# Optimization experiments

Hardware: AMD Instinct MI355X
Metric: run time of the kernel (lower is better)

The kernel has to match this reference:

```python
import jax, jax.numpy as jnp
import numpy as np

NUM_EXPERTS = 8
IN_FEATURES = 1024
OUT_FEATURES = 1024
TOTAL_TOKENS = 8192


def setup_inputs() -> dict:
    key = jax.random.key(0)
    k_x, k_w, k_b = jax.random.split(key, 3)
    inputs = jax.random.normal(k_x, (TOTAL_TOKENS, IN_FEATURES), dtype=jnp.float32)
    # lecun_normal-style scale for the per-expert kernels
    kernel = jax.random.normal(k_w, (NUM_EXPERTS, IN_FEATURES, OUT_FEATURES), dtype=jnp.float32) / np.sqrt(IN_FEATURES)
    bias = jax.random.normal(k_b, (NUM_EXPERTS, OUT_FEATURES), dtype=jnp.float32) * 0.01
    # ragged group sizes that sum exactly to TOTAL_TOKENS (tokens pre-sorted by expert)
    rng = np.random.default_rng(0)
    gs = rng.multinomial(TOTAL_TOKENS, [1.0 / NUM_EXPERTS] * NUM_EXPERTS)
    group_sizes = jnp.asarray(gs, dtype=jnp.int32)
    return {"inputs": inputs, "group_sizes": group_sizes, "kernel": kernel, "bias": bias}


def reference(inputs, group_sizes, kernel, bias):
    # inputs: [T, in], kernel: [E, in, out], bias: [E, out], group_sizes: [E]
    E = kernel.shape[0]
    T = inputs.shape[0]
    # per-token expert id (tokens are sorted/grouped by expert)
    expert_ids = jnp.repeat(jnp.arange(E, dtype=jnp.int32), group_sizes, total_repeat_length=T)  # [T]
    onehot = jax.nn.one_hot(expert_ids, E, dtype=inputs.dtype)  # [T, E]
    # grouped ragged matmul: y[t] = x[t] @ W[expert_ids[t]]
    xe = jnp.einsum("te,ti->eti", onehot, inputs)  # [E, T, in], zero outside each expert's group
    y = jnp.einsum("eti,eio->to", xe, kernel)  # [T, out]
    # ragged bias expansion: bias of the owning expert per token
    y = y + jnp.take(bias, expert_ids, axis=0)
    return y
```

## Files before the change

### kernel.cpp

```cpp
#include <hip/hip_runtime.h>
#include <hip/hip_bf16.h>

#define KDIM 1024
#define NDIM 1024
#define NEXP 8
#define TTOK 8192

typedef __bf16 bf16x8 __attribute__((ext_vector_type(8)));
typedef __bf16 bf16x4 __attribute__((ext_vector_type(4)));
typedef float  f32x4  __attribute__((ext_vector_type(4)));

__device__ __forceinline__ void gl2lds16(const void* g, void* l) {
  __builtin_amdgcn_global_load_lds(
      (const __attribute__((address_space(1))) void*)g,
      (__attribute__((address_space(3))) void*)l, 16, 0, 0);
}


__global__ __launch_bounds__(256) void prepass(
    const float* __restrict__ x, const float* __restrict__ W,
    __bf16* __restrict__ swA, __bf16* __restrict__ swB)
{
  __shared__ __align__(16) __bf16 Lt[64 * 72];
  const int t = threadIdx.x;
  if (blockIdx.x < 1024) {
#pragma unroll
    for (int p = 0; p < 4; ++p) {
      int s = blockIdx.x * 1024 + p * 256 + t;
      int lane = s & 63, kt = (s >> 6) & 31, panel = s >> 11;
      int row = panel * 16 + (lane & 15);
      int k0 = kt * 32 + ((lane >> 4) << 3);
      const float* xp = x + (size_t)row * KDIM + k0;
      float4 a = *(const float4*)xp;
      float4 b = *(const float4*)(xp + 4);
      bf16x8 v;
      v[0] = (__bf16)a.x; v[1] = (__bf16)a.y; v[2] = (__bf16)a.z; v[3] = (__bf16)a.w;
      v[4] = (__bf16)b.x; v[5] = (__bf16)b.y; v[6] = (__bf16)b.z; v[7] = (__bf16)b.w;
      *(bf16x8*)(swA + (size_t)s * 8) = v;
    }
  } else {
    int bid = blockIdx.x - 1024;
    int e = bid >> 8, r = bid & 255;
    int k0 = (r >> 4) * 64, n0 = (r & 15) * 64;
    const float* Wp = W + (size_t)e * KDIM * NDIM;
    int rr0 = t >> 4, c4 = t & 15;
#pragma unroll
    for (int p = 0; p < 4; ++p) {
      int kk = rr0 + p * 16;
      float4 v = *(const float4*)(Wp + (size_t)(k0 + kk) * NDIM + n0 + c4 * 4);
      Lt[(c4 * 4 + 0) * 72 + kk] = (__bf16)v.x;
      Lt[(c4 * 4 + 1) * 72 + kk] = (__bf16)v.y;
      Lt[(c4 * 4 + 2) * 72 + kk] = (__bf16)v.z;
      Lt[(c4 * 4 + 3) * 72 + kk] = (__bf16)v.w;
    }
    __syncthreads();
#pragma unroll
    for (int q = 0; q < 2; ++q) {
      int slot = q * 256 + t;
      int lane = slot & 63, grp = slot >> 6;
      int np = grp & 3, kt2 = grp >> 2;
      int nl = np * 16 + (lane & 15);
      int kl = kt2 * 32 + ((lane >> 4) << 3);
      bf16x8 v = *(const bf16x8*)(Lt + nl * 72 + kl);
      int panel = (n0 >> 4) + np;
      int ktg = (k0 >> 5) + kt2;
      size_t sg = (((size_t)e * 64 + panel) * 32 + ktg) * 64 + lane;
      *(bf16x8*)(swB + sg * 8) = v;
    }
  }
}

__global__ __launch_bounds__(256, 3) void moe_gemm_lds(
    const __bf16* __restrict__ swA, const __bf16* __restrict__ swB,
    const int* __restrict__ gs, const float* __restrict__ bias,
    float* __restrict__ out)
{
  __shared__ __align__(16) __bf16 buf[3][8192];

  int y = blockIdx.y;
  int e = 0, tile0 = 0, lo = 0, hi = 0, found = 0, off = 0;
#pragma unroll
  for (int i = 0; i < NEXP; ++i) {
    int g = gs[i];
    int first = off >> 7;
    int cnt = (g > 0) ? (((off + g - 1) >> 7) - first + 1) : 0;
    if (!found) {
      if (y < cnt) {
        found = 1; e = i; tile0 = (first + y) << 7;
        lo = max(tile0, off); hi = min(tile0 + 128, off + g);
      } else y -= cnt;
    }
    off += g;
  }
  if (!found) return;
  const int n0 = blockIdx.x * 128;

  const int t = threadIdx.x, lane = t & 63, wv = t >> 6;
  const int wm = wv & 1, wn = wv >> 1, lm = lane & 15, lg = lane >> 4;

  const __bf16* gA0 = swA + (size_t)((tile0 >> 4) + wv) * 16384 + lane * 8;
  const __bf16* gA1 = swA + (size_t)((tile0 >> 4) + 4 + wv) * 16384 + lane * 8;
  const __bf16* gB0 = swB + (size_t)(e * 64 + (n0 >> 4) + wv) * 16384 + lane * 8;
  const __bf16* gB1 = swB + (size_t)(e * 64 + (n0 >> 4) + 4 + wv) * 16384 + lane * 8;

  auto stage = [&](int kt, int sb) {
    __bf16* l = &buf[sb][0];
    const int ko = kt * 512;
    gl2lds16(gA0 + ko, l + (size_t)(0 * 256 + wv * 64) * 8);
    gl2lds16(gA1 + ko, l + (size_t)(1 * 256 + wv * 64) * 8);
    gl2lds16(gB0 + ko, l + (size_t)(2 * 256 + wv * 64) * 8);
    gl2lds16(gB1 + ko, l + (size_t)(3 * 256 + wv * 64) * 8);
  };

  f32x4 acc[4][4] = {};
  auto compute = [&](const __bf16* l) {
    bf16x8 aF[4], bF[4];
#pragma unroll
    for (int i = 0; i < 4; ++i)
      aF[i] = *(const bf16x8*)(l + (size_t)((wm * 4 + i) * 64 + lane) * 8);
#pragma unroll
    for (int j = 0; j < 4; ++j)
      bF[j] = *(const bf16x8*)(l + 4096 + (size_t)((wn * 4 + j) * 64 + lane) * 8);
#pragma unroll
    for (int i = 0; i < 4; ++i)
#pragma unroll
      for (int j = 0; j < 4; ++j)
        acc[i][j] = __builtin_amdgcn_mfma_f32_16x16x32_bf16(aF[i], bF[j], acc[i][j], 0, 0, 0);
  };

  stage(0, 0);
  stage(1, 1);
#pragma unroll 1
  for (int kt = 0; kt < KDIM / 32 - 1; ++kt) {
    asm volatile("s_waitcnt vmcnt(4)" ::: "memory");
    asm volatile("s_barrier" ::: "memory");
    compute(&buf[kt % 3][0]);
    if (kt + 2 < KDIM / 32) stage(kt + 2, (kt + 2) % 3);
  }
  asm volatile("s_waitcnt vmcnt(0)" ::: "memory");
  asm volatile("s_barrier" ::: "memory");
  compute(&buf[(KDIM / 32 - 1) % 3][0]);

  float bj[4];
#pragma unroll
  for (int j = 0; j < 4; ++j) bj[j] = bias[e * NDIM + n0 + wn * 64 + j * 16 + lm];
#pragma unroll
  for (int i = 0; i < 4; ++i)
#pragma unroll
    for (int r = 0; r < 4; ++r) {
      int rabs = tile0 + wm * 64 + i * 16 + lg * 4 + r;
      if (rabs >= lo && rabs < hi) {
#pragma unroll
        for (int j = 0; j < 4; ++j)
          out[(size_t)rabs * NDIM + n0 + wn * 64 + j * 16 + lm] = acc[i][j][r] + bj[j];
      }
    }
}

#define LDA 40
__global__ __launch_bounds__(256) void moe_gemm_kernel(
    const float* __restrict__ x, const int* __restrict__ gs,
    const float* __restrict__ W, const float* __restrict__ bias,
    float* __restrict__ out)
{
  __shared__ __bf16 Al[128 * LDA];
  __shared__ __bf16 Bl[128 * LDA];
  const int e = blockIdx.z, mt = blockIdx.y, nt = blockIdx.x;
  int off = 0;
#pragma unroll
  for (int i = 0; i < NEXP; ++i) { int g = gs[i]; if (i < e) off += g; }
  const int ge = gs[e];
  const int m0 = mt * 128;
  if (m0 >= ge) return;
  const int rows = min(128, ge - m0);
  const int row0 = off + m0;
  const int n0 = nt * 128;
  const int t = threadIdx.x, lane = t & 63, wv = t >> 6;
  const int wm = wv & 1, wn = wv >> 1, lm = lane & 15, lg = lane >> 4;
  const int am = t >> 3, kq = t & 7, nb = t & 127, kh = t >> 7;
  float4 aReg[4]; float bReg[16];
  const float* Wp = W + (size_t)e * KDIM * NDIM + n0 + nb;
  auto load_tile = [&](int kt) {
#pragma unroll
    for (int p = 0; p < 4; ++p) {
      int r = am + 32 * p;
      if (r < rows) aReg[p] = *(const float4*)(x + (size_t)(row0 + r) * KDIM + kt * 32 + kq * 4);
      else aReg[p] = make_float4(0.f, 0.f, 0.f, 0.f);
    }
    const float* wp = Wp + (size_t)(kt * 32 + kh * 16) * NDIM;
#pragma unroll
    for (int j = 0; j < 16; ++j) bReg[j] = wp[(size_t)j * NDIM];
  };
  auto store_tile = [&]() {
#pragma unroll
    for (int p = 0; p < 4; ++p) {
      bf16x4 v;
      v[0] = (__bf16)aReg[p].x; v[1] = (__bf16)aReg[p].y;
      v[2] = (__bf16)aReg[p].z; v[3] = (__bf16)aReg[p].w;
      *(bf16x4*)(Al + (am + 32 * p) * LDA + kq * 4) = v;
    }
    bf16x8 b0, b1;
#pragma unroll
    for (int j = 0; j < 8; ++j) { b0[j] = (__bf16)bReg[j]; b1[j] = (__bf16)bReg[8 + j]; }
    *(bf16x8*)(Bl + nb * LDA + kh * 16) = b0;
    *(bf16x8*)(Bl + nb * LDA + kh * 16 + 8) = b1;
  };
  f32x4 acc[4][4] = {};
  load_tile(0);
#pragma unroll 1
  for (int kt = 0; kt < KDIM / 32; ++kt) {
    __syncthreads();
    store_tile();
    __syncthreads();
    if (kt + 1 < KDIM / 32) load_tile(kt + 1);
    bf16x8 af[4], bfr[4];
#pragma unroll
    for (int i = 0; i < 4; ++i)
      af[i] = *(const bf16x8*)(Al + (wm * 64 + i * 16 + lm) * LDA + lg * 8);
#pragma unroll
    for (int j = 0; j < 4; ++j)
      bfr[j] = *(const bf16x8*)(Bl + (wn * 64 + j * 16 + lm) * LDA + lg * 8);
#pragma unroll
    for (int i = 0; i < 4; ++i)
#pragma unroll
      for (int j = 0; j < 4; ++j)
        acc[i][j] = __builtin_amdgcn_mfma_f32_16x16x32_bf16(af[i], bfr[j], acc[i][j], 0, 0, 0);
  }
  float bj[4];
#pragma unroll
  for (int j = 0; j < 4; ++j) bj[j] = bias[e * NDIM + n0 + wn * 64 + j * 16 + lm];
#pragma unroll
  for (int i = 0; i < 4; ++i)
#pragma unroll
    for (int r = 0; r < 4; ++r) {
      int rr = wm * 64 + i * 16 + lg * 4 + r;
      if (rr < rows) {
#pragma unroll
        for (int j = 0; j < 4; ++j)
          out[(size_t)(row0 + rr) * NDIM + n0 + wn * 64 + j * 16 + lm] = acc[i][j][r] + bj[j];
      }
    }
}

extern "C" void kernel_launch(void* const* d_in, const int* in_sizes, int n_in,
                              void* d_out, int out_size, void* d_ws, size_t ws_size,
                              hipStream_t stream) {
  const float* x    = (const float*)d_in[0];
  const int*   gs   = (const int*)d_in[1];
  const float* W    = (const float*)d_in[2];
  const float* bias = (const float*)d_in[3];
  float*       out  = (float*)d_out;

  const size_t swA_bytes = (size_t)TTOK * KDIM * 2;
  const size_t swB_bytes = (size_t)NEXP * KDIM * NDIM * 2;
  if (ws_size >= swA_bytes + swB_bytes) {
    __bf16* swA = (__bf16*)d_ws;
    __bf16* swB = (__bf16*)((char*)d_ws + swA_bytes);
    prepass<<<dim3(1024 + 2048), 256, 0, stream>>>(x, W, swA, swB);
    moe_gemm_lds<<<dim3(NDIM / 128, 72), 256, 0, stream>>>(swA, swB, gs, bias, out);
  } else {
    moe_gemm_kernel<<<dim3(NDIM / 128, TTOK / 128, NEXP), 256, 0, stream>>>(x, gs, W, bias, out);
  }
}
```

Measured before the change: 138.0 us.

## Fuse activation bf16 conversion into GEMM mainloop, drop activation prepass

Removes the activation half of the prepass, which converted x to a swizzled bf16 workspace. The GEMM now loads fp32 x directly into registers one k-tile ahead, converts it to bf16 and writes it into LDS after the MFMA block, while B keeps using async global-to-LDS loads. This saves the 16MB bf16 write and its re-read plus part of a kernel's work. In exchange, each x tile is re-read in fp32 by all 8 N-column blocks, adding register pressure and extra LDS waits. It also adds setprio and sched_barrier hints around the compute block.

```diff
diff --git a/kernel.cpp b/kernel.cpp
--- a/kernel.cpp
+++ b/kernel.cpp
@@ -5,6 +5,7 @@
 #define NDIM 1024
 #define NEXP 8
 #define TTOK 8192
+#define NT (KDIM / 32)
 
 typedef __bf16 bf16x8 __attribute__((ext_vector_type(8)));
 typedef __bf16 bf16x4 __attribute__((ext_vector_type(4)));
@@ -17,61 +18,43 @@
 }
 
 
-__global__ __launch_bounds__(256) void prepass(
-    const float* __restrict__ x, const float* __restrict__ W,
-    __bf16* __restrict__ swA, __bf16* __restrict__ swB)
+__global__ __launch_bounds__(256) void prepass_w(
+    const float* __restrict__ W, __bf16* __restrict__ swB)
 {
   __shared__ __align__(16) __bf16 Lt[64 * 72];
   const int t = threadIdx.x;
-  if (blockIdx.x < 1024) {
-#pragma unroll
-    for (int p = 0; p < 4; ++p) {
-      int s = blockIdx.x * 1024 + p * 256 + t;
-      int lane = s & 63, kt = (s >> 6) & 31, panel = s >> 11;
-      int row = panel * 16 + (lane & 15);
-      int k0 = kt * 32 + ((lane >> 4) << 3);
-      const float* xp = x + (size_t)row * KDIM + k0;
-      float4 a = *(const float4*)xp;
-      float4 b = *(const float4*)(xp + 4);
-      bf16x8 v;
-      v[0] = (__bf16)a.x; v[1] = (__bf16)a.y; v[2] = (__bf16)a.z; v[3] = (__bf16)a.w;
-      v[4] = (__bf16)b.x; v[5] = (__bf16)b.y; v[6] = (__bf16)b.z; v[7] = (__bf16)b.w;
-      *(bf16x8*)(swA + (size_t)s * 8) = v;
-    }
-  } else {
-    int bid = blockIdx.x - 1024;
-    int e = bid >> 8, r = bid & 255;
-    int k0 = (r >> 4) * 64, n0 = (r & 15) * 64;
-    const float* Wp = W + (size_t)e * KDIM * NDIM;
-    int rr0 = t >> 4, c4 = t & 15;
-#pragma unroll
-    for (int p = 0; p < 4; ++p) {
-      int kk = rr0 + p * 16;
-      float4 v = *(const float4*)(Wp + (size_t)(k0 + kk) * NDIM + n0 + c4 * 4);
-      Lt[(c4 * 4 + 0) * 72 + kk] = (__bf16)v.x;
-      Lt[(c4 * 4 + 1) * 72 + kk] = (__bf16)v.y;
-      Lt[(c4 * 4 + 2) * 72 + kk] = (__bf16)v.z;
-      Lt[(c4 * 4 + 3) * 72 + kk] = (__bf16)v.w;
-    }
-    __syncthreads();
-#pragma unroll
-    for (int q = 0; q < 2; ++q) {
-      int slot = q * 256 + t;
-      int lane = slot & 63, grp = slot >> 6;
-      int np = grp & 3, kt2 = grp >> 2;
-      int nl = np * 16 + (lane & 15);
-      int kl = kt2 * 32 + ((lane >> 4) << 3);
-      bf16x8 v = *(const bf16x8*)(Lt + nl * 72 + kl);
-      int panel = (n0 >> 4) + np;
-      int ktg = (k0 >> 5) + kt2;
-      size_t sg = (((size_t)e * 64 + panel) * 32 + ktg) * 64 + lane;
-      *(bf16x8*)(swB + sg * 8) = v;
-    }
+  int bid = blockIdx.x;
+  int e = bid >> 8, r = bid & 255;
+  int k0 = (r >> 4) * 64, n0 = (r & 15) * 64;
+  const float* Wp = W + (size_t)e * KDIM * NDIM;
+  int rr0 = t >> 4, c4 = t & 15;
+#pragma unroll
+  for (int p = 0; p < 4; ++p) {
+    int kk = rr0 + p * 16;
+    float4 v = *(const float4*)(Wp + (size_t)(k0 + kk) * NDIM + n0 + c4 * 4);
+    Lt[(c4 * 4 + 0) * 72 + kk] = (__bf16)v.x;
+    Lt[(c4 * 4 + 1) * 72 + kk] = (__bf16)v.y;
+    Lt[(c4 * 4 + 2) * 72 + kk] = (__bf16)v.z;
+    Lt[(c4 * 4 + 3) * 72 + kk] = (__bf16)v.w;
+  }
+  __syncthreads();
+#pragma unroll
+  for (int q = 0; q < 2; ++q) {
+    int slot = q * 256 + t;
+    int lane = slot & 63, grp = slot >> 6;
+    int np = grp & 3, kt2 = grp >> 2;
+    int nl = np * 16 + (lane & 15);
+    int kl = kt2 * 32 + ((lane >> 4) << 3);
+    bf16x8 v = *(const bf16x8*)(Lt + nl * 72 + kl);
+    int panel = (n0 >> 4) + np;
+    int ktg = (k0 >> 5) + kt2;
+    size_t sg = (((size_t)e * 64 + panel) * 32 + ktg) * 64 + lane;
+    *(bf16x8*)(swB + sg * 8) = v;
   }
 }
 
 __global__ __launch_bounds__(256, 3) void moe_gemm_lds(
-    const __bf16* __restrict__ swA, const __bf16* __restrict__ swB,
+    const float* __restrict__ x, const __bf16* __restrict__ swB,
     const int* __restrict__ gs, const float* __restrict__ bias,
     float* __restrict__ out)
 {
@@ -98,18 +81,33 @@
   const int t = threadIdx.x, lane = t & 63, wv = t >> 6;
   const int wm = wv & 1, wn = wv >> 1, lm = lane & 15, lg = lane >> 4;
 
-  const __bf16* gA0 = swA + (size_t)((tile0 >> 4) + wv) * 16384 + lane * 8;
-  const __bf16* gA1 = swA + (size_t)((tile0 >> 4) + 4 + wv) * 16384 + lane * 8;
   const __bf16* gB0 = swB + (size_t)(e * 64 + (n0 >> 4) + wv) * 16384 + lane * 8;
   const __bf16* gB1 = swB + (size_t)(e * 64 + (n0 >> 4) + 4 + wv) * 16384 + lane * 8;
 
-  auto stage = [&](int kt, int sb) {
+  auto stage_B = [&](int kt, int sb) {
     __bf16* l = &buf[sb][0];
     const int ko = kt * 512;
-    gl2lds16(gA0 + ko, l + (size_t)(0 * 256 + wv * 64) * 8);
-    gl2lds16(gA1 + ko, l + (size_t)(1 * 256 + wv * 64) * 8);
-    gl2lds16(gB0 + ko, l + (size_t)(2 * 256 + wv * 64) * 8);
-    gl2lds16(gB1 + ko, l + (size_t)(3 * 256 + wv * 64) * 8);
+    gl2lds16(gB0 + ko, l + (size_t)(512 + wv * 64) * 8);
+    gl2lds16(gB1 + ko, l + (size_t)(768 + wv * 64) * 8);
+  };
+
+  const float* xbase = x + (size_t)(tile0 + (t >> 3)) * KDIM + (t & 7) * 4;
+  const int abase = (((t >> 7) * 64 + ((t & 7) >> 1) * 16 + ((t >> 3) & 15)) << 3) + (t & 1) * 4;
+
+  auto issue_x = [&](int kt, float4* R) {
+#pragma unroll
+    for (int i = 0; i < 4; ++i)
+      R[i] = *(const float4*)(xbase + (size_t)i * 32 * KDIM + kt * 32);
+  };
+  auto write_A = [&](int sb, const float4* R) {
+    __bf16* l = &buf[sb][0] + abase;
+#pragma unroll
+    for (int i = 0; i < 4; ++i) {
+      bf16x4 b;
+      b[0] = (__bf16)R[i].x; b[1] = (__bf16)R[i].y;
+      b[2] = (__bf16)R[i].z; b[3] = (__bf16)R[i].w;
+      *(bf16x4*)(l + i * 1024) = b;
+    }
   };
 
   f32x4 acc[4][4] = {};
@@ -128,18 +126,37 @@
         acc[i][j] = __builtin_amdgcn_mfma_f32_16x16x32_bf16(aF[i], bF[j], acc[i][j], 0, 0, 0);
   };
 
-  stage(0, 0);
-  stage(1, 1);
+  {
+    float4 R0[4];
+    issue_x(0, R0);
+    stage_B(0, 0);
+    stage_B(1, 1);
+    asm volatile("s_waitcnt vmcnt(4)" ::: "memory");
+    write_A(0, R0);
+  }
+
 #pragma unroll 1
-  for (int kt = 0; kt < KDIM / 32 - 1; ++kt) {
-    asm volatile("s_waitcnt vmcnt(4)" ::: "memory");
+  for (int kt = 0; kt < NT; ++kt) {
+    asm volatile("s_waitcnt vmcnt(2)" ::: "memory");
+    asm volatile("s_waitcnt lgkmcnt(0)" ::: "memory");
     asm volatile("s_barrier" ::: "memory");
+
+    float4 R[4];
+    const bool havex = (kt + 1 < NT);
+    if (havex) issue_x(kt + 1, R);
+    if (kt + 2 < NT) stage_B(kt + 2, (kt + 2) % 3);
+    __builtin_amdgcn_sched_barrier(0);
+
+    __builtin_amdgcn_s_setprio(1);
     compute(&buf[kt % 3][0]);
-    if (kt + 2 < KDIM / 32) stage(kt + 2, (kt + 2) % 3);
-  }
-  asm volatile("s_waitcnt vmcnt(0)" ::: "memory");
-  asm volatile("s_barrier" ::: "memory");
-  compute(&buf[(KDIM / 32 - 1) % 3][0]);
+    __builtin_amdgcn_s_setprio(0);
+
+    if (havex) {
+      if (kt + 2 < NT) asm volatile("s_waitcnt vmcnt(2)" ::: "memory");
+      else             asm volatile("s_waitcnt vmcnt(0)" ::: "memory");
+      write_A((kt + 1) % 3, R);
+    }
+  }
 
   float bj[4];
 #pragma unroll
@@ -251,13 +268,11 @@
   const float* bias = (const float*)d_in[3];
   float*       out  = (float*)d_out;
 
-  const size_t swA_bytes = (size_t)TTOK * KDIM * 2;
   const size_t swB_bytes = (size_t)NEXP * KDIM * NDIM * 2;
-  if (ws_size >= swA_bytes + swB_bytes) {
-    __bf16* swA = (__bf16*)d_ws;
-    __bf16* swB = (__bf16*)((char*)d_ws + swA_bytes);
-    prepass<<<dim3(1024 + 2048), 256, 0, stream>>>(x, W, swA, swB);
-    moe_gemm_lds<<<dim3(NDIM / 128, 72), 256, 0, stream>>>(swA, swB, gs, bias, out);
+  if (ws_size >= swB_bytes) {
+    __bf16* swB = (__bf16*)d_ws;
+    prepass_w<<<dim3(2048), 256, 0, stream>>>(W, swB);
+    moe_gemm_lds<<<dim3(NDIM / 128, 72), 256, 0, stream>>>(x, swB, gs, bias, out);
   } else {
     moe_gemm_kernel<<<dim3(NDIM / 128, TTOK / 128, NEXP), 256, 0, stream>>>(x, gs, W, bias, out);
   }
```

Result: slower. 148.3 us (+7.5%).
